# Optimization experiments

Measured on AMD Instinct MI355X. Metric: run time of the kernel, lower is better.

The kernel has to match this reference:

```python
import jax, jax.numpy as jnp
import numpy as np

K = 5
PAD = 2  # same-size output: pad = dilation*(k-1)/2


def _patches(x, k, pad):
    # x: [B, C, H, W] -> [B, C, k, k, H', W'] (matches torch F.unfold + view layout)
    B, C, H, W = x.shape
    p = jax.lax.conv_general_dilated_patches(
        x, (k, k), (1, 1), [(pad, pad), (pad, pad)])
    return p.reshape(B, C, k, k, p.shape[-2], p.shape[-1])


def setup_inputs() -> dict:
    key = jax.random.key(0)
    k1, k2, k3, k4 = jax.random.split(key, 4)
    B, Cin, Cout, Cg, H, W = 4, 32, 32, 8, 128, 128
    x = jax.random.normal(k1, (B, Cin, H, W), jnp.float32)
    guide = jax.random.normal(k2, (B, Cg, H, W), jnp.float32)
    weight = jax.random.normal(k3, (Cout, Cin, K, K), jnp.float32) * 0.05
    bias = jax.random.normal(k4, (Cout,), jnp.float32) * 0.05
    return {"x": x, "guide": guide, "weight": weight, "bias": bias}


def reference(x, guide, weight, bias):
    k = weight.shape[-1]
    # --- packernel2d (gaussian, smooth_kernel_type='none', channel_wise=False) ---
    gp = _patches(guide, k, PAD)                      # [B, Cg, k, k, H, W]
    center = gp[:, :, k // 2, k // 2][:, :, None, None]  # self-tap feature
    d = gp - center
    kernel = jnp.exp(-0.5 * jnp.sum(d * d, axis=1, keepdims=True))  # [B,1,k,k,H,W]
    # --- pacconv2d native path ---
    cols = _patches(x, k, PAD)                        # [B, Cin, k, k, H, W]
    out = jnp.einsum('bjklmn,ojkl->bomn', cols * kernel, weight)
    return out + bias[None, :, None, None]
```

## Files before the change

### kernel.cpp

```cpp
#include <hip/hip_runtime.h>

#define Bn   4
#define CIN  32
#define COUT 32
#define CG   8
#define Hh   128
#define Ww   128
#define KK   5
#define HW   (Hh * Ww)

#define TW   64
#define TH   4
#define PRW  68
#define PRH  8
#define NSLOT (PRW * PRH)

typedef _Float16 h8  __attribute__((ext_vector_type(8)));
typedef _Float16 h2  __attribute__((ext_vector_type(2)));
typedef float    f4  __attribute__((ext_vector_type(4)));

#define XOFF  0
#define XJG   8704
#define WOFF  34816
#define KOFF  60416
#define SMEMB 73216

#define XT_OFF 0
#define WT_OFF 4194304
#define KW_OFF 4245504
#define WS_NEED 7522304

__global__ __launch_bounds__(512) void prep(
    const float* __restrict__ x, const float* __restrict__ guide,
    const float* __restrict__ w,
    _Float16* __restrict__ xt, _Float16* __restrict__ wt, _Float16* __restrict__ kw)
{
    const int bid = blockIdx.x;
    const int tid = threadIdx.x;

    if (bid < 512) {
        const int b = bid >> 7, m = bid & 127;
        const int n = tid & 127, jh = tid >> 7;
        const float* xp = x + ((size_t)(b * CIN + jh * 8)) * HW + m * Ww + n;
        h8 v;
#pragma unroll
        for (int e = 0; e < 8; ++e) v[e] = (_Float16)xp[(size_t)e * HW];
        ((h8*)xt)[((size_t)b * HW + m * Ww + n) * 4 + jh] = v;
    } else if (bid < 562) {
        const int idx = (bid - 512) * 512 + tid;
        const int ht = idx >> 9;
        const int half = ht / 25, t = ht - half * 25;
        const int rem = idx & 511;
        const int jg = rem >> 7, o = (rem >> 3) & 15, e = rem & 7;
        wt[idx] = (_Float16)w[(size_t)(half * 16 + o) * (CIN * KK * KK) + (jg * 8 + e) * (KK * KK) + t];
    } else {
        __shared__ __align__(16) _Float16 gl[NSLOT * 8];
        const int tb = bid - 562;
        const int tile = tb & 63, b = tb >> 6;
        const int tm = (tile >> 1) * TH, tn = (tile & 1) * TW;
        const float* gb = guide + (size_t)b * CG * HW;
#pragma unroll
        for (int it = 0; it < 2; ++it) {
            const int slot = it * 512 + tid;
            if (slot < NSLOT) {
                const int r = slot / PRW, c = slot - r * PRW;
                const int gm = tm + r - 2, gn = tn + c - 2;
                h8 v = {};
                if ((unsigned)gm < (unsigned)Hh && (unsigned)gn < (unsigned)Ww) {
#pragma unroll
                    for (int cg = 0; cg < 8; ++cg)
                        v[cg] = (_Float16)gb[(size_t)cg * HW + gm * Ww + gn];
                }
                *(h8*)(gl + slot * 8) = v;
            }
        }
        __syncthreads();
        const int px = tid & 255, th = tid >> 8;
        const int pr = px >> 6, pc = px & 63;
        const int pg = px >> 5, ps = (px >> 4) & 1, pi = px & 15;
        const h8 c8 = *(const h8*)(gl + ((pr + 2) * PRW + pc + 2) * 8);
        float cg[8];
#pragma unroll
        for (int i = 0; i < 8; ++i) cg[i] = (float)c8[i];
        _Float16* kout = kw + ((size_t)(b * 64 + tile) * 25) * 256;
        int t = 0;
#pragma unroll
        for (int k = 0; k < KK; ++k) {
#pragma unroll
            for (int l = 0; l < KK; ++l) {
                if ((t < 13) == (th == 0)) {
                    const h8 gv = *(const h8*)(gl + ((pr + k) * PRW + pc + l) * 8);
                    float ss = 0.f;
#pragma unroll
                    for (int i = 0; i < 8; ++i) {
                        const float d = (float)gv[i] - cg[i];
                        ss = fmaf(d, d, ss);
                    }
                    kout[t * 256 + (pg * 16 + pi) * 2 + ps] = (_Float16)__expf(-0.5f * ss);
                }
                ++t;
            }
        }
    }
}

__global__ __launch_bounds__(512, 2) void pac_mfma6(
    const _Float16* __restrict__ xt, const _Float16* __restrict__ wt,
    const _Float16* __restrict__ kw, const float* __restrict__ bias,
    float* __restrict__ out)
{
    __shared__ __align__(16) unsigned char smem[SMEMB];

    const int tid = threadIdx.x;
    const int bx  = blockIdx.x;
    const int bz  = blockIdx.y;
    const int tm = (bx >> 1) * TH;
    const int tn = (bx & 1) * TW;

    const int lane = tid & 63;
    const int l15 = lane & 15, kg = lane >> 4;

    const h8* wh1 = (const h8*)wt + 1600;
    h8 B1r[25];
#pragma unroll
    for (int t = 0; t < 25; ++t)
        B1r[t] = wh1[t * 64 + kg * 16 + l15];

    const int pxbase = bz * HW;
#pragma unroll
    for (int it = 0; it < 5; ++it) {
        const int idx = it * 512 + tid;
        if (idx < 2176) {
            const int slot = idx >> 2, jg = idx & 3;
            const int r = slot / PRW;
            const int c = slot - r * PRW;
            const int gm = tm + r - 2, gn = tn + c - 2;
            h8 v = {};
            if ((unsigned)gm < (unsigned)Hh && (unsigned)gn < (unsigned)Ww)
                v = *(const h8*)(xt + ((size_t)(pxbase + gm * Ww + gn)) * 32 + jg * 8);
            *(h8*)(smem + XOFF + jg * XJG + slot * 16) = v;
        }
    }

    const h8* wth = (const h8*)wt;
#pragma unroll
    for (int it = 0; it < 4; ++it) {
        const int idx = it * 512 + tid;
        if (idx < 1600)
            *(h8*)(smem + WOFF + idx * 16) = wth[idx];
    }

    const h8* ksrc = (const h8*)(kw + ((size_t)(bz * 64 + bx) * 25) * 256);
#pragma unroll
    for (int it = 0; it < 2; ++it) {
        const int idx = it * 512 + tid;
        if (idx < 800)
            *(h8*)(smem + KOFF + idx * 16) = ksrc[idx];
    }

    __syncthreads();

    const int wv = tid >> 6;
    const int st0 = wv * 32, st1 = st0 + 16;
    const int r0 = wv >> 1;
    const int c00 = (wv & 1) * 32;

    f4 acc00 = {0.f,0.f,0.f,0.f}, acc01 = {0.f,0.f,0.f,0.f};
    f4 acc10 = {0.f,0.f,0.f,0.f}, acc11 = {0.f,0.f,0.f,0.f};
    const unsigned char* xg = smem + XOFF + kg * XJG;
    const int kbase = KOFF + (wv * 16 + l15) * 4;

    int t = 0;
#pragma unroll
    for (int k = 0; k < KK; ++k) {
#pragma unroll
        for (int l = 0; l < KK; ++l) {
            const int abase = ((r0 + k) * PRW + c00 + l + l15) * 16;
            h8 A0 = *(const h8*)(xg + abase);
            h8 A1 = *(const h8*)(xg + abase + 256);
            h8 B0 = *(const h8*)(smem + WOFF + t * 1024 + kg * 256 + l15 * 16);
            h2 kk = *(const h2*)(smem + kbase + t * 512);

            h8 A0s = A0 * kk[0];
            h8 A1s = A1 * kk[1];

            acc00 = __builtin_amdgcn_mfma_f32_16x16x32_f16(A0s, B0,      acc00, 0, 0, 0);
            acc01 = __builtin_amdgcn_mfma_f32_16x16x32_f16(A0s, B1r[t],  acc01, 0, 0, 0);
            acc10 = __builtin_amdgcn_mfma_f32_16x16x32_f16(A1s, B0,      acc10, 0, 0, 0);
            acc11 = __builtin_amdgcn_mfma_f32_16x16x32_f16(A1s, B1r[t],  acc11, 0, 0, 0);
            ++t;
        }
    }

    const float bv0 = bias[l15], bv1 = bias[16 + l15];
#pragma unroll
    for (int i = 0; i < 4; ++i) {
        acc00[i] += bv0; acc10[i] += bv0;
        acc01[i] += bv1; acc11[i] += bv1;
    }

    __syncthreads();
    float* outst = (float*)smem;
    *(f4*)(outst + l15 * 260 + st0 + kg * 4) = acc00;
    *(f4*)(outst + l15 * 260 + st1 + kg * 4) = acc10;
    *(f4*)(outst + (16 + l15) * 260 + st0 + kg * 4) = acc01;
    *(f4*)(outst + (16 + l15) * 260 + st1 + kg * 4) = acc11;
    __syncthreads();

    const int o = tid >> 4;
    const int i = tid & 15;
    float* op = out + ((size_t)(bz * COUT + o)) * HW;
#pragma unroll
    for (int c = 0; c < 4; ++c) {
        f4 v = *(const f4*)(outst + o * 260 + c * 64 + i * 4);
        *(f4*)(op + (size_t)(tm + c) * Ww + tn + i * 4) = v;
    }
}

typedef _Float16 h4v __attribute__((ext_vector_type(4)));
__global__ __launch_bounds__(512, 4) void pac_mfma2(
    const float* __restrict__ x, const float* __restrict__ guide,
    const float* __restrict__ weight, const float* __restrict__ bias,
    float* __restrict__ out)
{
    __shared__ __align__(16) unsigned char smem[SMEMB];
    const int tid  = threadIdx.x;
    const int bx   = blockIdx.x;
    const int half = blockIdx.y;
    const int bz   = blockIdx.z;
    const int tm = (bx >> 1) * TH;
    const int tn = (bx & 1) * TW;

    const float* xb = x + (size_t)bz * CIN * HW;
#pragma unroll
    for (int it = 0; it < 34; ++it) {
        const int idx  = it * 512 + tid;
        const int j    = idx / NSLOT;
        const int slot = idx - j * NSLOT;
        const int r    = slot / PRW;
        const int c    = slot - r * PRW;
        const int gm = tm + r - 2, gn = tn + c - 2;
        float v = 0.f;
        if ((unsigned)gm < (unsigned)Hh && (unsigned)gn < (unsigned)Ww)
            v = xb[(size_t)j * HW + gm * Ww + gn];
        *(_Float16*)(smem + XOFF + (j >> 3) * XJG + slot * 16 + (j & 7) * 2) = (_Float16)v;
    }
#pragma unroll
    for (int it = 0; it < 25; ++it) {
        const int idx = it * 512 + tid;
        const int o = idx & 15;
        const int j = (idx >> 4) & 31;
        const int t = idx >> 9;
        const float v = weight[(size_t)(half * 16 + o) * (CIN * KK * KK) + j * (KK * KK) + t];
        *(_Float16*)(smem + WOFF + t * 1024 + (j >> 3) * 256 + o * 16 + (j & 7) * 2) = (_Float16)v;
    }
    {
        const int px = tid & 255, th = tid >> 8;
        const int pr = px >> 6, pc = px & 63;
        const int m = tm + pr, n = tn + pc;
        const float* gb = guide + ((size_t)bz * CG) * HW + m * Ww + n;
        float center[CG];
#pragma unroll
        for (int c = 0; c < CG; ++c) center[c] = gb[c * HW];
        int t = 0;
#pragma unroll
        for (int k = 0; k < KK; ++k) {
            const int dm = k - 2;
            const bool rowok = ((unsigned)(m + dm) < (unsigned)Hh);
#pragma unroll
            for (int l = 0; l < KK; ++l) {
                if ((t < 13) == (th == 0)) {
                    const int dn = l - 2;
                    const bool ok = rowok && ((unsigned)(n + dn) < (unsigned)Ww);
                    float ss = 0.f;
#pragma unroll
                    for (int c = 0; c < CG; ++c) {
                        float gv = ok ? gb[c * HW + dm * Ww + dn] : 0.f;
                        float d = gv - center[c];
                        ss = fmaf(d, d, ss);
                    }
                    *(_Float16*)(smem + KOFF + t * 512 + px * 2) = (_Float16)__expf(-0.5f * ss);
                }
                ++t;
            }
        }
    }
    __syncthreads();
    const int lane = tid & 63;
    const int l15 = lane & 15, kg = lane >> 4;
    const int wv = tid >> 6;
    const int st0 = wv * 32, st1 = st0 + 16;
    const int r0 = wv >> 1;
    const int c00 = (wv & 1) * 32;
    f4 acc0 = {0.f, 0.f, 0.f, 0.f}, acc1 = {0.f, 0.f, 0.f, 0.f};
    const unsigned char* xg = smem + XOFF + kg * XJG;
    const float bv = bias[half * 16 + l15];
    int t = 0;
#pragma unroll
    for (int k = 0; k < KK; ++k) {
#pragma unroll
        for (int l = 0; l < KK; ++l) {
            const int abase = ((r0 + k) * PRW + c00 + l + l15) * 16;
            h8 A0 = *(const h8*)(xg + abase);
            h8 A1 = *(const h8*)(xg + abase + 256);
            h8 Bv = *(const h8*)(smem + WOFF + t * 1024 + kg * 256 + l15 * 16);
            f4 p0 = __builtin_amdgcn_mfma_f32_16x16x32_f16(A0, Bv, (f4){0.f,0.f,0.f,0.f}, 0, 0, 0);
            f4 p1 = __builtin_amdgcn_mfma_f32_16x16x32_f16(A1, Bv, (f4){0.f,0.f,0.f,0.f}, 0, 0, 0);
            h4v k0 = *(const h4v*)(smem + KOFF + t * 512 + (st0 + kg * 4) * 2);
            h4v k1 = *(const h4v*)(smem + KOFF + t * 512 + (st1 + kg * 4) * 2);
#pragma unroll
            for (int i = 0; i < 4; ++i) {
                acc0[i] = fmaf((float)k0[i], p0[i], acc0[i]);
                acc1[i] = fmaf((float)k1[i], p1[i], acc1[i]);
            }
            ++t;
        }
    }
#pragma unroll
    for (int i = 0; i < 4; ++i) { acc0[i] += bv; acc1[i] += bv; }
    __syncthreads();
    float* outst = (float*)smem;
    *(f4*)(outst + l15 * 260 + st0 + kg * 4) = acc0;
    *(f4*)(outst + l15 * 260 + st1 + kg * 4) = acc1;
    __syncthreads();
    const int o = tid >> 5;
    const int p = (tid & 31) * 8;
    f4 v0 = *(const f4*)(outst + o * 260 + p);
    f4 v1 = *(const f4*)(outst + o * 260 + p + 4);
    const int mr = p >> 6, nc = p & 63;
    float* op = out + ((size_t)(bz * COUT + half * 16 + o)) * HW + (size_t)(tm + mr) * Ww + tn + nc;
    *(f4*)op = v0;
    *(f4*)(op + 4) = v1;
}

extern "C" void kernel_launch(void* const* d_in, const int* in_sizes, int n_in,
                              void* d_out, int out_size, void* d_ws, size_t ws_size,
                              hipStream_t stream) {
    const float* x      = (const float*)d_in[0];
    const float* guide  = (const float*)d_in[1];
    const float* weight = (const float*)d_in[2];
    const float* bias   = (const float*)d_in[3];
    float* out = (float*)d_out;

    if (ws_size >= (size_t)WS_NEED) {
        _Float16* xt = (_Float16*)((char*)d_ws + XT_OFF);
        _Float16* wt = (_Float16*)((char*)d_ws + WT_OFF);
        _Float16* kw = (_Float16*)((char*)d_ws + KW_OFF);
        prep<<<dim3(818), 512, 0, stream>>>(x, guide, weight, xt, wt, kw);
        pac_mfma6<<<dim3(64, Bn), 512, 0, stream>>>(xt, wt, kw, bias, out);
    } else {
        pac_mfma2<<<dim3(64, 2, Bn), 512, 0, stream>>>(x, guide, weight, bias, out);
    }
}
```

Baseline: 23.60 us.

## Fuse guide-kernel exponential computation into main MFMA kernel

The prep kernel now only transposes the guide into a channel-packed fp16 layout instead of computing the 25-tap Gaussian weights. The main kernel computes those weights itself from global memory and writes them straight into shared memory. This removes the precomputed weight buffer's write and read round trip and shrinks the prep grid. In exchange, the main kernel does extra uncached neighbour gathers and exp math before its MFMA loop, which could lengthen its prologue.

```diff
diff --git a/kernel.cpp b/kernel.cpp
--- a/kernel.cpp
+++ b/kernel.cpp
@@ -27,13 +27,13 @@
 
 #define XT_OFF 0
 #define WT_OFF 4194304
-#define KW_OFF 4245504
-#define WS_NEED 7522304
+#define GT_OFF 4245504
+#define WS_NEED 5294080
 
 __global__ __launch_bounds__(512) void prep(
     const float* __restrict__ x, const float* __restrict__ guide,
     const float* __restrict__ w,
-    _Float16* __restrict__ xt, _Float16* __restrict__ wt, _Float16* __restrict__ kw)
+    _Float16* __restrict__ xt, _Float16* __restrict__ wt, _Float16* __restrict__ gt)
 {
     const int bid = blockIdx.x;
     const int tid = threadIdx.x;
@@ -54,59 +54,20 @@
         const int jg = rem >> 7, o = (rem >> 3) & 15, e = rem & 7;
         wt[idx] = (_Float16)w[(size_t)(half * 16 + o) * (CIN * KK * KK) + (jg * 8 + e) * (KK * KK) + t];
     } else {
-        __shared__ __align__(16) _Float16 gl[NSLOT * 8];
-        const int tb = bid - 562;
-        const int tile = tb & 63, b = tb >> 6;
-        const int tm = (tile >> 1) * TH, tn = (tile & 1) * TW;
-        const float* gb = guide + (size_t)b * CG * HW;
-#pragma unroll
-        for (int it = 0; it < 2; ++it) {
-            const int slot = it * 512 + tid;
-            if (slot < NSLOT) {
-                const int r = slot / PRW, c = slot - r * PRW;
-                const int gm = tm + r - 2, gn = tn + c - 2;
-                h8 v = {};
-                if ((unsigned)gm < (unsigned)Hh && (unsigned)gn < (unsigned)Ww) {
-#pragma unroll
-                    for (int cg = 0; cg < 8; ++cg)
-                        v[cg] = (_Float16)gb[(size_t)cg * HW + gm * Ww + gn];
-                }
-                *(h8*)(gl + slot * 8) = v;
-            }
-        }
-        __syncthreads();
-        const int px = tid & 255, th = tid >> 8;
-        const int pr = px >> 6, pc = px & 63;
-        const int pg = px >> 5, ps = (px >> 4) & 1, pi = px & 15;
-        const h8 c8 = *(const h8*)(gl + ((pr + 2) * PRW + pc + 2) * 8);
-        float cg[8];
-#pragma unroll
-        for (int i = 0; i < 8; ++i) cg[i] = (float)c8[i];
-        _Float16* kout = kw + ((size_t)(b * 64 + tile) * 25) * 256;
-        int t = 0;
-#pragma unroll
-        for (int k = 0; k < KK; ++k) {
-#pragma unroll
-            for (int l = 0; l < KK; ++l) {
-                if ((t < 13) == (th == 0)) {
-                    const h8 gv = *(const h8*)(gl + ((pr + k) * PRW + pc + l) * 8);
-                    float ss = 0.f;
-#pragma unroll
-                    for (int i = 0; i < 8; ++i) {
-                        const float d = (float)gv[i] - cg[i];
-                        ss = fmaf(d, d, ss);
-                    }
-                    kout[t * 256 + (pg * 16 + pi) * 2 + ps] = (_Float16)__expf(-0.5f * ss);
-                }
-                ++t;
-            }
-        }
+        const int gr = (bid - 562) * 4 + (tid >> 7);
+        const int b = gr >> 7, m = gr & 127;
+        const int n = tid & 127;
+        const float* gp = guide + ((size_t)b * CG) * HW + m * Ww + n;
+        h8 v;
+#pragma unroll
+        for (int e = 0; e < 8; ++e) v[e] = (_Float16)gp[(size_t)e * HW];
+        ((h8*)gt)[(size_t)b * HW + m * Ww + n] = v;
     }
 }
 
-__global__ __launch_bounds__(512, 2) void pac_mfma6(
+__global__ __launch_bounds__(512, 2) void pac_mfma7(
     const _Float16* __restrict__ xt, const _Float16* __restrict__ wt,
-    const _Float16* __restrict__ kw, const float* __restrict__ bias,
+    const _Float16* __restrict__ gt, const float* __restrict__ bias,
     float* __restrict__ out)
 {
     __shared__ __align__(16) unsigned char smem[SMEMB];
@@ -150,12 +111,38 @@
             *(h8*)(smem + WOFF + idx * 16) = wth[idx];
     }
 
-    const h8* ksrc = (const h8*)(kw + ((size_t)(bz * 64 + bx) * 25) * 256);
-#pragma unroll
-    for (int it = 0; it < 2; ++it) {
-        const int idx = it * 512 + tid;
-        if (idx < 800)
-            *(h8*)(smem + KOFF + idx * 16) = ksrc[idx];
+    {
+        const int px = tid & 255, th = tid >> 8;
+        const int pr = px >> 6, pc = px & 63;
+        const int pg = px >> 5, ps = (px >> 4) & 1, pi = px & 15;
+        const int m = tm + pr, n = tn + pc;
+        const h8* gtb = (const h8*)gt + (size_t)bz * HW;
+        const h8 c8 = gtb[m * Ww + n];
+        float cg[8];
+#pragma unroll
+        for (int i = 0; i < 8; ++i) cg[i] = (float)c8[i];
+        int t = 0;
+#pragma unroll
+        for (int k = 0; k < KK; ++k) {
+#pragma unroll
+            for (int l = 0; l < KK; ++l) {
+                if ((t < 13) == (th == 0)) {
+                    const int gm = m + k - 2, gn = n + l - 2;
+                    h8 gv = {};
+                    if ((unsigned)gm < (unsigned)Hh && (unsigned)gn < (unsigned)Ww)
+                        gv = gtb[gm * Ww + gn];
+                    float ss = 0.f;
+#pragma unroll
+                    for (int i = 0; i < 8; ++i) {
+                        const float d = (float)gv[i] - cg[i];
+                        ss = fmaf(d, d, ss);
+                    }
+                    *(_Float16*)(smem + KOFF + t * 512 + ((pg * 16 + pi) * 2 + ps) * 2) =
+                        (_Float16)__expf(-0.5f * ss);
+                }
+                ++t;
+            }
+        }
     }
 
     __syncthreads();
@@ -184,10 +171,10 @@
             h8 A0s = A0 * kk[0];
             h8 A1s = A1 * kk[1];
 
-            acc00 = __builtin_amdgcn_mfma_f32_16x16x32_f16(A0s, B0,      acc00, 0, 0, 0);
-            acc01 = __builtin_amdgcn_mfma_f32_16x16x32_f16(A0s, B1r[t],  acc01, 0, 0, 0);
-            acc10 = __builtin_amdgcn_mfma_f32_16x16x32_f16(A1s, B0,      acc10, 0, 0, 0);
-            acc11 = __builtin_amdgcn_mfma_f32_16x16x32_f16(A1s, B1r[t],  acc11, 0, 0, 0);
+            acc00 = __builtin_amdgcn_mfma_f32_16x16x32_f16(A0s, B0,     acc00, 0, 0, 0);
+            acc01 = __builtin_amdgcn_mfma_f32_16x16x32_f16(A0s, B1r[t], acc01, 0, 0, 0);
+            acc10 = __builtin_amdgcn_mfma_f32_16x16x32_f16(A1s, B0,     acc10, 0, 0, 0);
+            acc11 = __builtin_amdgcn_mfma_f32_16x16x32_f16(A1s, B1r[t], acc11, 0, 0, 0);
             ++t;
         }
     }
@@ -345,9 +332,9 @@
     if (ws_size >= (size_t)WS_NEED) {
         _Float16* xt = (_Float16*)((char*)d_ws + XT_OFF);
         _Float16* wt = (_Float16*)((char*)d_ws + WT_OFF);
-        _Float16* kw = (_Float16*)((char*)d_ws + KW_OFF);
-        prep<<<dim3(818), 512, 0, stream>>>(x, guide, weight, xt, wt, kw);
-        pac_mfma6<<<dim3(64, Bn), 512, 0, stream>>>(xt, wt, kw, bias, out);
+        _Float16* gt = (_Float16*)((char*)d_ws + GT_OFF);
+        prep<<<dim3(690), 512, 0, stream>>>(x, guide, weight, xt, wt, gt);
+        pac_mfma7<<<dim3(64, Bn), 512, 0, stream>>>(xt, wt, gt, bias, out);
     } else {
         pac_mfma2<<<dim3(64, 2, Bn), 512, 0, stream>>>(x, guide, weight, bias, out);
     }
```

Measured after the change: 23.28 us (median of 2 runs). No clear change (-1.4%).
